# Kernel tuning notes

Hardware: AMD Instinct MI355X
Metric: run time of the kernel (lower is better)

## Reference

```python
import jax, jax.numpy as jnp
import numpy as np

B, OBS, H, M, L1, T, A = 16384, 376, 512, 8, 3, 50, 17  # L1 = num_layers - 1
LOG_SQRT_2PI = 0.5 * np.log(2.0 * np.pi).astype(np.float32)


def setup_inputs() -> dict:
    key = jax.random.key(0)
    ks = jax.random.split(key, 16)
    s = lambda fan: 1.0 / np.sqrt(fan).astype(np.float32)
    return {
        "x": jax.random.normal(ks[0], (B, OBS), jnp.float32),
        "task_idx": jax.random.randint(ks[1], (B,), 0, T, jnp.int64),
        "enc_W1": jax.random.normal(ks[2], (OBS, H), jnp.float32) * s(OBS),
        "enc_b1": jnp.zeros((H,), jnp.float32),
        "enc_W2": jax.random.normal(ks[3], (H, H), jnp.float32) * s(H),
        "enc_b2": jnp.zeros((H,), jnp.float32),
        "task_emb": jax.random.normal(ks[4], (T, H), jnp.float32),
        "a_rW": jax.random.normal(ks[5], (L1, H, M * M), jnp.float32) * s(H),
        "a_rb": jnp.zeros((L1, M * M), jnp.float32),
        "c_rW": jax.random.normal(ks[6], (L1, H, M * M), jnp.float32) * s(H),
        "c_rb": jnp.zeros((L1, M * M), jnp.float32),
        "a_W": jax.random.normal(ks[7], (L1, M, H, H), jnp.float32) * s(H),
        "a_b": jnp.zeros((L1, M, H), jnp.float32),
        "a_Wf": jax.random.normal(ks[8], (M, H, A), jnp.float32) * 0.01,
        "a_bf": jnp.zeros((M, A), jnp.float32),
        "c_W": jax.random.normal(ks[9], (L1, M, H, H), jnp.float32) * s(H),
        "c_b": jnp.zeros((L1, M, H), jnp.float32),
        "c_Wf": jax.random.normal(ks[10], (M, H, 1), jnp.float32) * s(H),
        "c_bf": jnp.zeros((M, 1), jnp.float32),
        "actor_logstd": jnp.zeros((1, A), jnp.float32),
    }


def _routing(context, rW, rb):
    # context: [B,H]; rW: [L1,H,M*M] -> list of [B,M,M] softmax routing probs
    rel = jax.nn.relu(context)
    probs = []
    for l in range(L1):
        logits = (rel @ rW[l] + rb[l]).reshape(-1, M, M)
        probs.append(jax.nn.softmax(logits, axis=2))
    return probs


def _base(f_s, probs, W, b, Wf, bf):
    # f_s: [B,H]; W: [L1,M,H,H]; Wf: [M,H,out]
    g = jnp.broadcast_to(f_s[:, None, :], (f_s.shape[0], M, H))  # [B,M,H]
    for l in range(L1):
        outs = jax.nn.relu(jnp.einsum("bmh,mhk->bmk", g, W[l]) + b[l])  # [B,M,H]
        g = jnp.einsum("bij,bjh->bih", probs[l], outs)  # soft combine
    final = jnp.einsum("bmh,mhk->bmk", g, Wf) + bf  # [B,M,out]
    return final.sum(axis=1)


def reference(x, task_idx, enc_W1, enc_b1, enc_W2, enc_b2, task_emb,
              a_rW, a_rb, c_rW, c_rb, a_W, a_b, a_Wf, a_bf,
              c_W, c_b, c_Wf, c_bf, actor_logstd):
    f_s = jnp.tanh(jnp.tanh(x @ enc_W1 + enc_b1) @ enc_W2 + enc_b2)  # [B,H]
    h_z = task_emb[task_idx]  # [B,H]
    context = f_s * h_z

    value = _base(f_s, _routing(context, c_rW, c_rb), c_W, c_b, c_Wf, c_bf)  # [B,1]
    mean = _base(f_s, _routing(context, a_rW, a_rb), a_W, a_b, a_Wf, a_bf)   # [B,A]

    # deterministic action (sample=False): action = mean
    logstd = jnp.broadcast_to(actor_logstd, mean.shape)
    log_prob = (-logstd - LOG_SQRT_2PI).sum(axis=1)          # N.log_prob(mean).sum(1)
    entropy = (0.5 + LOG_SQRT_2PI + logstd).sum(axis=1)
    # concat (action, log_prob, entropy, value) -> [B, A+3]
    return jnp.concatenate([mean, log_prob[:, None], entropy[:, None], value], axis=1)
```

## Files before the change

kernel.cpp:

```cpp
#include <hip/hip_runtime.h>
#include <hip/hip_bf16.h>

typedef float f32x4 __attribute__((ext_vector_type(4)));
typedef float f32x2 __attribute__((ext_vector_type(2)));
typedef int   i32x4 __attribute__((ext_vector_type(4)));
typedef int   i32x8 __attribute__((ext_vector_type(8)));

#define LOG_SQRT_2PI 0.91893853320467274f

static constexpr int BSZ  = 16384;
static constexpr int OBSN = 376;
static constexpr int HD   = 512;
static constexpr int NACT = 17;

__device__ __forceinline__ unsigned char f2fp8(float v) {
  return (unsigned char)(__builtin_amdgcn_cvt_pk_fp8_f32(v, v, 0, false) & 0xFF);
}

__device__ __forceinline__ void gl16(const unsigned char* g, unsigned char* l) {
  __builtin_amdgcn_global_load_lds((const __attribute__((address_space(1))) void*)g,
                                   (__attribute__((address_space(3))) void*)l, 16, 0, 0);
}

__device__ __forceinline__ void xcd_map(int id, int gx, int gy, int& bx, int& by, int& bz) {
  int p = id & 7, l = id >> 3;
  bx = l % gx;
  int g = (l / gx) * 8 + p;
  by = g % gy;
  bz = g / gy;
}


__global__ void k_cvt_pad8(const float* __restrict__ src, unsigned char* __restrict__ dst) {
  long i = (long)blockIdx.x * 256 + threadIdx.x;
  if (i >= (long)BSZ * HD) return;
  long r = i >> 9;
  int  c = (int)(i & 511);
  dst[i] = f2fp8(c < OBSN ? src[r * OBSN + c] : 0.f);
}

__global__ void k_packT8(const float* __restrict__ src, unsigned char* __restrict__ dst,
                         int K, int N, int Kpad, long sstride, long dstride, float scale) {
  __shared__ float t[32][33];
  src += (long)blockIdx.z * sstride;
  dst += (long)blockIdx.z * dstride;
  int k0 = blockIdx.y * 32, n0 = blockIdx.x * 32;
#pragma unroll
  for (int ii = 0; ii < 4; ++ii) {
    int i = ii * 8 + threadIdx.y;
    int k = k0 + i, n = n0 + threadIdx.x;
    t[i][threadIdx.x] = (k < K && n < N) ? src[(long)k * N + n] : 0.f;
  }
  __syncthreads();
#pragma unroll
  for (int ii = 0; ii < 4; ++ii) {
    int i = ii * 8 + threadIdx.y;
    int n = n0 + i, k = k0 + threadIdx.x;
    if (n < N && k < Kpad) dst[(long)n * Kpad + k] = f2fp8(scale * t[threadIdx.x][i]);
  }
}

__global__ void k_packwF(const float* __restrict__ aW, const float* __restrict__ cW,
                         unsigned char* __restrict__ dst) {
  __shared__ unsigned char sT[128 * 144];
  const int tid = threadIdx.x;
  const int z = blockIdx.z;
  const int t = blockIdx.y;
  const int ng = blockIdx.x;
  const int layer = z >> 4, zz = z & 15, net = zz >> 3, m = zz & 7;
  const float* src = (net ? aW : cW) + (long)(layer * 8 + m) * 262144;
#pragma unroll
  for (int i = 0; i < 64; ++i) {
    int lin = i * 256 + tid;
    int kl = lin >> 7, nl = lin & 127;
    float v = src[(long)(t * 128 + kl) * 512 + ng * 128 + nl];
    sT[nl * 144 + kl] = f2fp8(16.f * v);
  }
  __syncthreads();
#pragma unroll
  for (int f = 0; f < 2; ++f) {
    int fid = f * 256 + tid;
    int lane = fid & 63, nb_l = fid >> 6;
    int n_l = nb_l * 16 + (lane & 15);
    int klo = ((lane >> 4) & 3) * 32;
    uint4 lo = *(const uint4*)&sT[n_l * 144 + klo];
    uint4 hi = *(const uint4*)&sT[n_l * 144 + klo + 16];
    int nb = ng * 8 + nb_l;
    unsigned char* d = dst + ((((long)z * 4 + t) * 32 + nb) * 64 + lane) * 32;
    *(uint4*)d = lo;
    *(uint4*)(d + 16) = hi;
  }
}

__global__ void k_packmisc(const float* __restrict__ a_b, const float* __restrict__ c_b,
                           const float* __restrict__ aWf, const float* __restrict__ cWf,
                           const float* __restrict__ a_rb, const float* __restrict__ c_rb,
                           float* __restrict__ lb, unsigned char* __restrict__ dsta,
                           unsigned char* __restrict__ dstc, float* __restrict__ rb) {
  int i = blockIdx.x * 256 + threadIdx.x;
  if (i < 24576) {
    int layer = i >> 13, zz = (i >> 9) & 15, n = i & 511;
    int net = zz >> 3, m = zz & 7;
    lb[i] = (net ? a_b : c_b)[(layer * 8 + m) * 512 + n];
  } else if (i < 24576 + 131072) {
    int j = i - 24576;
    int n = j >> 12, kn = j & 4095;
    int hb = kn >> 9, rem = kn & 511, m = rem >> 6, u = kn & 63;
    int ko = m * 512 + hb * 64 + u;
    dsta[j] = (n < NACT) ? f2fp8(64.f * aWf[(long)ko * NACT + n]) : (unsigned char)0;
    dstc[j] = (n < 1)    ? f2fp8(64.f * cWf[ko])                  : (unsigned char)0;
  } else if (i < 24576 + 131072 + 384) {
    int j = i - 24576 - 131072;
    rb[j] = (j < 192) ? a_rb[j] : c_rb[j - 192];
  }
}

__global__ void k_initout2(const float* __restrict__ a_bf, const float* __restrict__ c_bf,
                           const float* __restrict__ ls, float* __restrict__ out) {
  long i = (long)blockIdx.x * 256 + threadIdx.x;
  if (i >= (long)BSZ * 20) return;
  int o = (int)(i % 20);
  float v = 0.f;
  if (o < NACT) {
    for (int m = 0; m < 8; ++m) v += a_bf[m * NACT + o];
  } else if (o == 19) {
    for (int m = 0; m < 8; ++m) v += c_bf[m];
  } else if (o == 17) {
    for (int a = 0; a < NACT; ++a) v += -ls[a] - LOG_SQRT_2PI;
  } else {
    for (int a = 0; a < NACT; ++a) v += 0.5f + LOG_SQRT_2PI + ls[a];
  }
  out[i] = v;
}

template <int OP>
__global__ __launch_bounds__(256, 4)
void k_gemm8(const unsigned char* __restrict__ A, const unsigned char* __restrict__ Bt,
             void* __restrict__ Cv, const float* __restrict__ bias,
             int N, int K, int lda, int ldc, int gx, int gy,
             const int* __restrict__ tidx, const float* __restrict__ temb,
             unsigned char* __restrict__ out2) {
  __shared__ alignas(16) unsigned char sA[128 * 128];
  __shared__ alignas(16) unsigned char sB[128 * 128];
  int bx, by, z;
  xcd_map(blockIdx.x, gx, gy, bx, by, z);
  const int tid  = threadIdx.x;
  const int wave = tid >> 6, lane = tid & 63;
  const int wr = (wave >> 1) * 64, wc = (wave & 1) * 64;
  const int row0 = by * 128, col0 = bx * 128;
  const int lcol = lane & 15, quad = lane >> 4;
  const int sw7 = lcol & 7;
  const int c0 = ((2 * quad)     ^ sw7) * 16;
  const int c1 = ((2 * quad + 1) ^ sw7) * 16;
  const int raA0 = (wr + lcol) * 128 + c0, raA1 = (wr + lcol) * 128 + c1;
  const int rbB0 = (wc + lcol) * 128 + c0, rbB1 = (wc + lcol) * 128 + c1;
  int aOff[4], bOff[4];
#pragma unroll
  for (int i = 0; i < 4; ++i) {
    int u = i * 256 + tid;
    int r = u >> 3, gc = (u & 7) ^ (r & 7);
    aOff[i] = (row0 + r) * lda + gc * 16;
    bOff[i] = (col0 + r) * K + gc * 16;
  }

  f32x4 acc[4][4] = {};

  for (int kt = 0; kt < K; kt += 128) {
#pragma unroll
    for (int i = 0; i < 4; ++i) gl16(A + aOff[i] + kt, &sA[i * 4096 + tid * 16]);
#pragma unroll
    for (int i = 0; i < 4; ++i) gl16(Bt + bOff[i] + kt, &sB[i * 4096 + tid * 16]);
    __syncthreads();
    i32x8 bv[4];
#pragma unroll
    for (int ni = 0; ni < 4; ++ni) {
      i32x4 blo = *(const i32x4*)&sB[rbB0 + ni * 2048];
      i32x4 bhi = *(const i32x4*)&sB[rbB1 + ni * 2048];
      bv[ni] = (i32x8){blo[0], blo[1], blo[2], blo[3], bhi[0], bhi[1], bhi[2], bhi[3]};
    }
#pragma unroll
    for (int mi = 0; mi < 4; ++mi) {
      i32x4 alo = *(const i32x4*)&sA[raA0 + mi * 2048];
      i32x4 ahi = *(const i32x4*)&sA[raA1 + mi * 2048];
      i32x8 af = (i32x8){alo[0], alo[1], alo[2], alo[3], ahi[0], ahi[1], ahi[2], ahi[3]};
#pragma unroll
      for (int ni = 0; ni < 4; ++ni)
        acc[mi][ni] = __builtin_amdgcn_mfma_scale_f32_16x16x128_f8f6f4(
            bv[ni], af, acc[mi][ni], 0, 0, 0, 0x7F, 0, 0x7F);
    }
    __syncthreads();
  }

#pragma unroll
  for (int ni = 0; ni < 4; ++ni) {
    int colb = col0 + wc + ni * 16 + quad * 4;
    if (colb >= N) continue;
    float4 bw = *(const float4*)&bias[colb];
#pragma unroll
    for (int mi = 0; mi < 4; ++mi) {
      int rowg = row0 + wr + mi * 16 + lcol;
      float v0 = acc[mi][ni][0] * 0.0625f + bw.x;
      float v1 = acc[mi][ni][1] * 0.0625f + bw.y;
      float v2 = acc[mi][ni][2] * 0.0625f + bw.z;
      float v3 = acc[mi][ni][3] * 0.0625f + bw.w;
      long idx = (long)rowg * ldc + colb;
      if (OP == 1) {
        float t0 = tanhf(v0), t1 = tanhf(v1), t2 = tanhf(v2), t3 = tanhf(v3);
        unsigned d = __builtin_amdgcn_cvt_pk_fp8_f32(t0, t1, 0, false);
        d = __builtin_amdgcn_cvt_pk_fp8_f32(t2, t3, d, true);
        *(unsigned*)&((unsigned char*)Cv)[idx] = d;
      } else if (OP == 5) {
        float t0 = tanhf(v0), t1 = tanhf(v1), t2 = tanhf(v2), t3 = tanhf(v3);
        unsigned d = __builtin_amdgcn_cvt_pk_fp8_f32(t0, t1, 0, false);
        d = __builtin_amdgcn_cvt_pk_fp8_f32(t2, t3, d, true);
        *(unsigned*)&((unsigned char*)Cv)[idx] = d;
        int tk = tidx[rowg];
        float4 te = *(const float4*)&temb[(long)tk * HD + colb];
        unsigned e = __builtin_amdgcn_cvt_pk_fp8_f32(fmaxf(t0 * te.x, 0.f), fmaxf(t1 * te.y, 0.f), 0, false);
        e = __builtin_amdgcn_cvt_pk_fp8_f32(fmaxf(t2 * te.z, 0.f), fmaxf(t3 * te.w, 0.f), e, true);
        *(unsigned*)&out2[idx] = e;
      } else if (OP == 4) {
        float mx = fmaxf(fmaxf(v0, v1), fmaxf(v2, v3));
        mx = fmaxf(mx, __shfl_xor(mx, 16));
        float e0 = __expf(v0 - mx), e1 = __expf(v1 - mx), e2 = __expf(v2 - mx), e3 = __expf(v3 - mx);
        float s = e0 + e1 + e2 + e3;
        s += __shfl_xor(s, 16);
        float inv = 1.f / s;
        *(float4*)&((float*)Cv)[idx] = make_float4(e0 * inv, e1 * inv, e2 * inv, e3 * inv);
      }
    }
  }
}

template <int AMODE, int HEAD>
__global__ __launch_bounds__(512, 4)
void k_gemmF(const unsigned char* __restrict__ A, const unsigned char* __restrict__ Wp,
             const float* __restrict__ lb, const float* __restrict__ probs,
             unsigned char* __restrict__ g, int gy, int poffC, int poffA,
             const unsigned char* __restrict__ Wfc, const unsigned char* __restrict__ Wfa,
             float* __restrict__ outp) {
  __shared__ alignas(16) unsigned char sL[AMODE ? 65536 : 32768];
  int hb, slab, net;
  xcd_map(blockIdx.x, 8, gy, hb, slab, net);
  const int tid = threadIdx.x;
  const int w = tid >> 6, lane = tid & 63;
  const int lcol = lane & 15, quad = lane >> 4;
  const int ln3 = lane >> 3, sl = lane & 7;
  const int row0 = slab * 64;
  const int h0 = hb * 64;
  const int sw7 = lcol & 7;
  const int c0 = ((2 * quad)     ^ sw7) * 16;
  const int c1 = ((2 * quad + 1) ^ sw7) * 16;
  const int ch = sl ^ ln3;
  const unsigned char* wbase =
      Wp + (((long)(net * 8 + w) * 4 * 32 + hb * 4) * 64 + lane) * 32;

  f32x4 acc[4][4] = {};

  if (AMODE == 0) {
#pragma unroll
    for (int i = 0; i < 4; ++i) {
      int vb = w * 4 + i;
      int rr = (vb & 7) * 8 + ln3;
      gl16(A + (row0 + rr) * 512 + (vb >> 3) * 128 + ch * 16, &sL[(vb * 64 + lane) * 16]);
    }
    __syncthreads();
#pragma unroll
    for (int t = 0; t < 4; ++t) {
      i32x8 bv[4];
#pragma unroll
      for (int ni = 0; ni < 4; ++ni) {
        i32x4 lo = *(const i32x4*)(wbase + t * 65536 + ni * 2048);
        i32x4 hi = *(const i32x4*)(wbase + t * 65536 + ni * 2048 + 16);
        bv[ni] = (i32x8){lo[0], lo[1], lo[2], lo[3], hi[0], hi[1], hi[2], hi[3]};
      }
      __builtin_amdgcn_s_setprio(1);
#pragma unroll
      for (int mi = 0; mi < 4; ++mi) {
        int ra = t * 8192 + (mi * 16 + lcol) * 128;
        i32x4 lo = *(const i32x4*)&sL[ra + c0];
        i32x4 hi = *(const i32x4*)&sL[ra + c1];
        i32x8 af = (i32x8){lo[0], lo[1], lo[2], lo[3], hi[0], hi[1], hi[2], hi[3]};
#pragma unroll
        for (int ni = 0; ni < 4; ++ni)
          acc[mi][ni] = __builtin_amdgcn_mfma_scale_f32_16x16x128_f8f6f4(
              bv[ni], af, acc[mi][ni], 0, 0, 0, 0x7F, 0, 0x7F);
      }
      __builtin_amdgcn_s_setprio(0);
    }
  } else {
    const unsigned char* abase = A + (long)(row0 + ln3) * 8192 + net * 4096 +
                                 w * 64 + (ch >> 2) * 512 + (ch & 3) * 16;
    unsigned char* dbase = &sL[w * 8192 + lane * 16];
#pragma unroll 1
    for (int t = 0; t < 4; ++t) {
#pragma unroll
      for (int i = 0; i < 8; ++i)
        gl16(abase + i * 8 * 8192 + t * 1024, dbase + i * 1024);
      i32x8 bv[4];
#pragma unroll
      for (int ni = 0; ni < 4; ++ni) {
        i32x4 lo = *(const i32x4*)(wbase + t * 65536 + ni * 2048);
        i32x4 hi = *(const i32x4*)(wbase + t * 65536 + ni * 2048 + 16);
        bv[ni] = (i32x8){lo[0], lo[1], lo[2], lo[3], hi[0], hi[1], hi[2], hi[3]};
      }
      asm volatile("s_waitcnt vmcnt(0)" ::: "memory");
      __builtin_amdgcn_sched_barrier(0);
      __builtin_amdgcn_s_setprio(1);
#pragma unroll
      for (int mi = 0; mi < 4; ++mi) {
        int ra = w * 8192 + (mi * 16 + lcol) * 128;
        i32x4 lo = *(const i32x4*)&sL[ra + c0];
        i32x4 hi = *(const i32x4*)&sL[ra + c1];
        i32x8 af = (i32x8){lo[0], lo[1], lo[2], lo[3], hi[0], hi[1], hi[2], hi[3]};
#pragma unroll
        for (int ni = 0; ni < 4; ++ni)
          acc[mi][ni] = __builtin_amdgcn_mfma_scale_f32_16x16x128_f8f6f4(
              bv[ni], af, acc[mi][ni], 0, 0, 0, 0x7F, 0, 0x7F);
      }
      __builtin_amdgcn_s_setprio(0);
    }
  }

  __syncthreads();

#pragma unroll
  for (int ni = 0; ni < 4; ++ni) {
    int col = ni * 16 + quad * 4;
    float4 bw = *(const float4*)&lb[(net * 8 + w) * 512 + h0 + col];
    int sd = ni * 4 + quad;
#pragma unroll
    for (int mi = 0; mi < 4; ++mi) {
      int row = mi * 16 + lcol;
      float v0 = fmaxf(acc[mi][ni][0] * 0.0625f + bw.x, 0.f);
      float v1 = fmaxf(acc[mi][ni][1] * 0.0625f + bw.y, 0.f);
      float v2 = fmaxf(acc[mi][ni][2] * 0.0625f + bw.z, 0.f);
      float v3 = fmaxf(acc[mi][ni][3] * 0.0625f + bw.w, 0.f);
      unsigned d = __builtin_amdgcn_cvt_pk_fp8_f32(v0, v1, 0, false);
      d = __builtin_amdgcn_cvt_pk_fp8_f32(v2, v3, d, true);
      *(unsigned*)&sL[w * 4096 + row * 64 + ((sd ^ (row & 14)) << 2)] = d;
    }
  }
  __syncthreads();

  const int poff = net ? poffA : poffC;
#pragma unroll
  for (int k = 0; k < 8; ++k) {
    const int r = k * 8 + ln3;
    const float* pr = &probs[(long)(row0 + r) * 384 + poff + w * 8];
    float4 pA = *(const float4*)pr;
    float4 pB = *(const float4*)(pr + 4);
    float p8[8] = {pA.x, pA.y, pA.z, pA.w, pB.x, pB.y, pB.z, pB.w};
    f32x2 ga2[4] = {};
#pragma unroll
    for (int j = 0; j < 8; ++j) {
      uint2 o2 = *(const uint2*)&sL[j * 4096 + r * 64 + (((sl * 2) ^ (r & 14)) << 2)];
      f32x2 pw2 = {p8[j], p8[j]};
      ga2[0] += pw2 * __builtin_amdgcn_cvt_pk_f32_fp8(o2.x, false);
      ga2[1] += pw2 * __builtin_amdgcn_cvt_pk_f32_fp8(o2.x, true);
      ga2[2] += pw2 * __builtin_amdgcn_cvt_pk_f32_fp8(o2.y, false);
      ga2[3] += pw2 * __builtin_amdgcn_cvt_pk_f32_fp8(o2.y, true);
    }
    unsigned lo = __builtin_amdgcn_cvt_pk_fp8_f32(ga2[0][0], ga2[0][1], 0, false);
    lo = __builtin_amdgcn_cvt_pk_fp8_f32(ga2[1][0], ga2[1][1], lo, true);
    unsigned hi = __builtin_amdgcn_cvt_pk_fp8_f32(ga2[2][0], ga2[2][1], 0, false);
    hi = __builtin_amdgcn_cvt_pk_fp8_f32(ga2[3][0], ga2[3][1], hi, true);
    if (HEAD) {
      *(uint2*)&sL[32768 + w * 4096 + r * 64 + (((sl * 2) ^ (r & 14)) << 2)] =
          make_uint2(lo, hi);
    } else {
      *(uint2*)&g[(long)(row0 + r) * 8192 + net * 4096 + hb * 512 + w * 64 + sl * 8] =
          make_uint2(lo, hi);
    }
  }

  if (HEAD) {
    __syncthreads();
    const unsigned char* Wf = net ? Wfa : Wfc;
    const int ooff = net ? 0 : 19;
    const int mi = w & 3, kh = w >> 2;
    const int hrow = mi * 16 + lcol;
    f32x4 hacc[2] = {};
#pragma unroll
    for (int ks = 0; ks < 8; ++ks) {
      int j = kh * 4 + (ks >> 1);
      int u = (ks & 1) * 32 + quad * 8;
      int sd = u >> 2;
      long af = *(const long*)&sL[32768 + j * 4096 + hrow * 64 + ((sd ^ (hrow & 14)) << 2)];
      int kglob = hb * 512 + kh * 256 + ks * 32 + quad * 8;
      long bv0 = *(const long*)&Wf[(long)lcol * 4096 + kglob];
      hacc[0] = __builtin_amdgcn_mfma_f32_16x16x32_fp8_fp8(af, bv0, hacc[0], 0, 0, 0);
      if (net) {
        long bv1 = *(const long*)&Wf[(long)(16 + lcol) * 4096 + kglob];
        hacc[1] = __builtin_amdgcn_mfma_f32_16x16x32_fp8_fp8(af, bv1, hacc[1], 0, 0, 0);
      }
    }
    const int NOUTn = net ? NACT : 1;
#pragma unroll
    for (int ni = 0; ni < 2; ++ni) {
      if (ni == 1 && !net) break;
      int col = ni * 16 + lcol;
      if (col >= NOUTn) continue;
#pragma unroll
      for (int rr = 0; rr < 4; ++rr) {
        int row = row0 + mi * 16 + quad * 4 + rr;
        atomicAdd(&outp[(long)row * 20 + ooff + col], hacc[ni][rr] * 0.015625f);
      }
    }
  }
}


extern "C" void kernel_launch(void* const* d_in, const int* in_sizes, int n_in,
                              void* d_out, int out_size, void* d_ws, size_t ws_size,
                              hipStream_t stream) {
  const float* x        = (const float*)d_in[0];
  const int*   task_idx = (const int*)d_in[1];
  const float* enc_W1   = (const float*)d_in[2];
  const float* enc_b1   = (const float*)d_in[3];
  const float* enc_W2   = (const float*)d_in[4];
  const float* enc_b2   = (const float*)d_in[5];
  const float* task_emb = (const float*)d_in[6];
  const float* a_rW     = (const float*)d_in[7];
  const float* a_rb     = (const float*)d_in[8];
  const float* c_rW     = (const float*)d_in[9];
  const float* c_rb     = (const float*)d_in[10];
  const float* a_W      = (const float*)d_in[11];
  const float* a_b      = (const float*)d_in[12];
  const float* a_Wf     = (const float*)d_in[13];
  const float* a_bf     = (const float*)d_in[14];
  const float* c_W      = (const float*)d_in[15];
  const float* c_b      = (const float*)d_in[16];
  const float* c_Wf     = (const float*)d_in[17];
  const float* c_bf     = (const float*)d_in[18];
  const float* logstd   = (const float*)d_in[19];
  float* out = (float*)d_out;

  char* ws = (char*)d_ws;
  size_t off = 0;
  auto carve = [&](size_t bytes) {
    char* p = ws + off;
    off += (bytes + 255) & ~(size_t)255;
    return p;
  };
  unsigned char* W8 = (unsigned char*)carve((size_t)48 * 262144);
  unsigned char* W1T8 = (unsigned char*)carve((size_t)512 * 512);
  unsigned char* W2T8 = (unsigned char*)carve((size_t)512 * 512);
  unsigned char* rWT8 = (unsigned char*)carve((size_t)384 * 512);
  float* rball = (float*)carve(384 * 4);
  float* lb    = (float*)carve(3 * 16 * 512 * 4);
  unsigned char* WfaT8 = (unsigned char*)carve((size_t)32 * 4096);
  unsigned char* WfcT8 = (unsigned char*)carve((size_t)32 * 4096);
  unsigned char* fs8 = (unsigned char*)carve((size_t)BSZ * HD);
  float* lgt   = (float*)carve((size_t)BSZ * 384 * 4);

  size_t remain = (ws_size > off) ? (ws_size - off) : 0;
  int Bc = 2048;
  for (int cand = BSZ; cand > 2048; cand >>= 1)
    if ((size_t)2 * cand * 8192 <= remain) { Bc = cand; break; }
  size_t half = (size_t)Bc * 8192;
  unsigned char* bufA8 = (unsigned char*)carve(half);
  unsigned char* bufB8 = (unsigned char*)carve(half);
  unsigned char* x8   = bufA8;
  unsigned char* h18  = bufB8;
  unsigned char* rel8 = bufA8;

  dim3 tb(32, 8);

  k_cvt_pad8<<<(int)(((long)BSZ * HD + 255) / 256), 256, 0, stream>>>(x, x8);
  k_packT8<<<dim3(16, 16, 1), tb, 0, stream>>>(enc_W1, W1T8, OBSN, 512, 512, 0, 0, 16.f);
  k_packT8<<<dim3(16, 16, 1), tb, 0, stream>>>(enc_W2, W2T8, 512, 512, 512, 0, 0, 16.f);
  k_packT8<<<dim3(2, 16, 3),  tb, 0, stream>>>(a_rW, rWT8,             512, 64, 512, 512 * 64, 64 * 512, 16.f);
  k_packT8<<<dim3(2, 16, 3),  tb, 0, stream>>>(c_rW, rWT8 + 192 * 512, 512, 64, 512, 512 * 64, 64 * 512, 16.f);
  k_packwF<<<dim3(4, 4, 48), 256, 0, stream>>>(a_W, c_W, W8);
  k_packmisc<<<610, 256, 0, stream>>>(a_b, c_b, a_Wf, c_Wf, a_rb, c_rb,
                                      lb, WfaT8, WfcT8, rball);
  k_initout2<<<(int)(((long)BSZ * 20 + 255) / 256), 256, 0, stream>>>(a_bf, c_bf, logstd, out);

  const int GY = BSZ / 128;
  k_gemm8<1><<<4 * GY, 256, 0, stream>>>(x8, W1T8, h18, enc_b1, 512, 512, 512, 512,
                                         4, GY, nullptr, nullptr, nullptr);
  k_gemm8<5><<<4 * GY, 256, 0, stream>>>(h18, W2T8, fs8, enc_b2, 512, 512, 512, 512,
                                         4, GY, task_idx, task_emb, rel8);
  k_gemm8<4><<<3 * GY, 256, 0, stream>>>(rel8, rWT8, lgt, rball, 384, 512, 512, 384,
                                         3, GY, nullptr, nullptr, nullptr);

  const size_t wlz = (size_t)16 * 262144;
  for (int c0 = 0; c0 < BSZ; c0 += Bc) {
    const unsigned char* fs_c = fs8 + (long)c0 * 512;
    const float* pr_c  = lgt + (long)c0 * 384;
    float*       out_c = out + (long)c0 * 20;
    const int gyF = Bc / 64;

    k_gemmF<0, 0><<<16 * gyF, 512, 0, stream>>>(fs_c, W8, lb, pr_c, bufA8, gyF, 192, 0,
                                                nullptr, nullptr, nullptr);
    k_gemmF<1, 0><<<16 * gyF, 512, 0, stream>>>(bufA8, W8 + wlz, lb + 8192, pr_c, bufB8,
                                                gyF, 192 + 64, 64, nullptr, nullptr, nullptr);
    k_gemmF<1, 1><<<16 * gyF, 512, 0, stream>>>(bufB8, W8 + 2 * wlz, lb + 16384, pr_c, bufA8,
                                                gyF, 192 + 128, 128, WfcT8, WfaT8, out_c);
  }
}
```

Before: 696.7 us.

## Halve row slab for later mixture layers to raise occupancy and change g layout

For layers 2 and 3 of the mixture network, each block now handles 32 rows instead of 64. This halves the LDS footprint to 32 KB and the accumulator registers, and the launch bound is raised to 6 blocks per CU so more waves stay resident. The intermediate g buffer layout changes from hb*512 + w*64 to w*512 + h0, making each expert's hidden vector contiguous so the layer loads become 128-byte contiguous chunks per expert. The trade-off is twice as many blocks and weight fetches per row, so each weight byte is reused less.

```diff
diff --git a/kernel.cpp b/kernel.cpp
--- a/kernel.cpp
+++ b/kernel.cpp
@@ -233,20 +233,20 @@
 }
 
 template <int AMODE, int HEAD>
-__global__ __launch_bounds__(512, 4)
+__global__ __launch_bounds__(512, AMODE ? 6 : 4)
 void k_gemmF(const unsigned char* __restrict__ A, const unsigned char* __restrict__ Wp,
              const float* __restrict__ lb, const float* __restrict__ probs,
              unsigned char* __restrict__ g, int gy, int poffC, int poffA,
              const unsigned char* __restrict__ Wfc, const unsigned char* __restrict__ Wfa,
              float* __restrict__ outp) {
-  __shared__ alignas(16) unsigned char sL[AMODE ? 65536 : 32768];
+  __shared__ alignas(16) unsigned char sL[32768];
   int hb, slab, net;
   xcd_map(blockIdx.x, 8, gy, hb, slab, net);
   const int tid = threadIdx.x;
   const int w = tid >> 6, lane = tid & 63;
   const int lcol = lane & 15, quad = lane >> 4;
   const int ln3 = lane >> 3, sl = lane & 7;
-  const int row0 = slab * 64;
+  const int row0 = slab * (AMODE ? 32 : 64);
   const int h0 = hb * 64;
   const int sw7 = lcol & 7;
   const int c0 = ((2 * quad)     ^ sw7) * 16;
@@ -254,10 +254,10 @@
   const int ch = sl ^ ln3;
   const unsigned char* wbase =
       Wp + (((long)(net * 8 + w) * 4 * 32 + hb * 4) * 64 + lane) * 32;
-
-  f32x4 acc[4][4] = {};
+  const int poff = net ? poffA : poffC;
 
   if (AMODE == 0) {
+    f32x4 acc[4][4] = {};
 #pragma unroll
     for (int i = 0; i < 4; ++i) {
       int vb = w * 4 + i;
@@ -288,40 +288,88 @@
       }
       __builtin_amdgcn_s_setprio(0);
     }
-  } else {
+    __syncthreads();
+
+#pragma unroll
+    for (int ni = 0; ni < 4; ++ni) {
+      int col = ni * 16 + quad * 4;
+      float4 bw = *(const float4*)&lb[(net * 8 + w) * 512 + h0 + col];
+      int sd = ni * 4 + quad;
+#pragma unroll
+      for (int mi = 0; mi < 4; ++mi) {
+        int row = mi * 16 + lcol;
+        float v0 = fmaxf(acc[mi][ni][0] * 0.0625f + bw.x, 0.f);
+        float v1 = fmaxf(acc[mi][ni][1] * 0.0625f + bw.y, 0.f);
+        float v2 = fmaxf(acc[mi][ni][2] * 0.0625f + bw.z, 0.f);
+        float v3 = fmaxf(acc[mi][ni][3] * 0.0625f + bw.w, 0.f);
+        unsigned d = __builtin_amdgcn_cvt_pk_fp8_f32(v0, v1, 0, false);
+        d = __builtin_amdgcn_cvt_pk_fp8_f32(v2, v3, d, true);
+        *(unsigned*)&sL[w * 4096 + row * 64 + ((sd ^ (row & 14)) << 2)] = d;
+      }
+    }
+    __syncthreads();
+
+#pragma unroll
+    for (int k = 0; k < 8; ++k) {
+      const int r = k * 8 + ln3;
+      const float* pr = &probs[(long)(row0 + r) * 384 + poff + w * 8];
+      float4 pA = *(const float4*)pr;
+      float4 pB = *(const float4*)(pr + 4);
+      float p8[8] = {pA.x, pA.y, pA.z, pA.w, pB.x, pB.y, pB.z, pB.w};
+      f32x2 ga2[4] = {};
+#pragma unroll
+      for (int j = 0; j < 8; ++j) {
+        uint2 o2 = *(const uint2*)&sL[j * 4096 + r * 64 + (((sl * 2) ^ (r & 14)) << 2)];
+        f32x2 pw2 = {p8[j], p8[j]};
+        ga2[0] += pw2 * __builtin_amdgcn_cvt_pk_f32_fp8(o2.x, false);
+        ga2[1] += pw2 * __builtin_amdgcn_cvt_pk_f32_fp8(o2.x, true);
+        ga2[2] += pw2 * __builtin_amdgcn_cvt_pk_f32_fp8(o2.y, false);
+        ga2[3] += pw2 * __builtin_amdgcn_cvt_pk_f32_fp8(o2.y, true);
+      }
+      unsigned lo = __builtin_amdgcn_cvt_pk_fp8_f32(ga2[0][0], ga2[0][1], 0, false);
+      lo = __builtin_amdgcn_cvt_pk_fp8_f32(ga2[1][0], ga2[1][1], lo, true);
+      unsigned hi = __builtin_amdgcn_cvt_pk_fp8_f32(ga2[2][0], ga2[2][1], 0, false);
+      hi = __builtin_amdgcn_cvt_pk_fp8_f32(ga2[3][0], ga2[3][1], hi, true);
+      *(uint2*)&g[(long)(row0 + r) * 8192 + net * 4096 + w * 512 + h0 + sl * 8] =
+          make_uint2(lo, hi);
+    }
+    return;
+  }
+
+  f32x4 acc[2][4] = {};
+  {
     const unsigned char* abase = A + (long)(row0 + ln3) * 8192 + net * 4096 +
-                                 w * 64 + (ch >> 2) * 512 + (ch & 3) * 16;
-    unsigned char* dbase = &sL[w * 8192 + lane * 16];
+                                 w * 512 + ch * 16;
+    unsigned char* dbase = &sL[w * 4096 + lane * 16];
 #pragma unroll 1
     for (int t = 0; t < 4; ++t) {
 #pragma unroll
-      for (int i = 0; i < 8; ++i)
-        gl16(abase + i * 8 * 8192 + t * 1024, dbase + i * 1024);
-      i32x8 bv[4];
+      for (int i = 0; i < 4; ++i)
+        gl16(abase + i * 8 * 8192 + t * 128, dbase + i * 1024);
+      asm volatile("s_waitcnt vmcnt(0)" ::: "memory");
+      __builtin_amdgcn_sched_barrier(0);
+      i32x8 af[2];
+#pragma unroll
+      for (int mi = 0; mi < 2; ++mi) {
+        int ra = w * 4096 + (mi * 16 + lcol) * 128;
+        i32x4 lo = *(const i32x4*)&sL[ra + c0];
+        i32x4 hi = *(const i32x4*)&sL[ra + c1];
+        af[mi] = (i32x8){lo[0], lo[1], lo[2], lo[3], hi[0], hi[1], hi[2], hi[3]};
+      }
+      __builtin_amdgcn_s_setprio(1);
 #pragma unroll
       for (int ni = 0; ni < 4; ++ni) {
         i32x4 lo = *(const i32x4*)(wbase + t * 65536 + ni * 2048);
         i32x4 hi = *(const i32x4*)(wbase + t * 65536 + ni * 2048 + 16);
-        bv[ni] = (i32x8){lo[0], lo[1], lo[2], lo[3], hi[0], hi[1], hi[2], hi[3]};
-      }
-      asm volatile("s_waitcnt vmcnt(0)" ::: "memory");
-      __builtin_amdgcn_sched_barrier(0);
-      __builtin_amdgcn_s_setprio(1);
-#pragma unroll
-      for (int mi = 0; mi < 4; ++mi) {
-        int ra = w * 8192 + (mi * 16 + lcol) * 128;
-        i32x4 lo = *(const i32x4*)&sL[ra + c0];
-        i32x4 hi = *(const i32x4*)&sL[ra + c1];
-        i32x8 af = (i32x8){lo[0], lo[1], lo[2], lo[3], hi[0], hi[1], hi[2], hi[3]};
-#pragma unroll
-        for (int ni = 0; ni < 4; ++ni)
-          acc[mi][ni] = __builtin_amdgcn_mfma_scale_f32_16x16x128_f8f6f4(
-              bv[ni], af, acc[mi][ni], 0, 0, 0, 0x7F, 0, 0x7F);
+        i32x8 bv = (i32x8){lo[0], lo[1], lo[2], lo[3], hi[0], hi[1], hi[2], hi[3]};
+        acc[0][ni] = __builtin_amdgcn_mfma_scale_f32_16x16x128_f8f6f4(
+            bv, af[0], acc[0][ni], 0, 0, 0, 0x7F, 0, 0x7F);
+        acc[1][ni] = __builtin_amdgcn_mfma_scale_f32_16x16x128_f8f6f4(
+            bv, af[1], acc[1][ni], 0, 0, 0, 0x7F, 0, 0x7F);
       }
       __builtin_amdgcn_s_setprio(0);
     }
   }
-
   __syncthreads();
 
 #pragma unroll
@@ -330,7 +378,7 @@
     float4 bw = *(const float4*)&lb[(net * 8 + w) * 512 + h0 + col];
     int sd = ni * 4 + quad;
 #pragma unroll
-    for (int mi = 0; mi < 4; ++mi) {
+    for (int mi = 0; mi < 2; ++mi) {
       int row = mi * 16 + lcol;
       float v0 = fmaxf(acc[mi][ni][0] * 0.0625f + bw.x, 0.f);
       float v1 = fmaxf(acc[mi][ni][1] * 0.0625f + bw.y, 0.f);
@@ -338,14 +386,13 @@
       float v3 = fmaxf(acc[mi][ni][3] * 0.0625f + bw.w, 0.f);
       unsigned d = __builtin_amdgcn_cvt_pk_fp8_f32(v0, v1, 0, false);
       d = __builtin_amdgcn_cvt_pk_fp8_f32(v2, v3, d, true);
-      *(unsigned*)&sL[w * 4096 + row * 64 + ((sd ^ (row & 14)) << 2)] = d;
+      *(unsigned*)&sL[w * 2048 + row * 64 + ((sd ^ (row & 14)) << 2)] = d;
     }
   }
   __syncthreads();
 
-  const int poff = net ? poffA : poffC;
-#pragma unroll
-  for (int k = 0; k < 8; ++k) {
+#pragma unroll
+  for (int k = 0; k < 4; ++k) {
     const int r = k * 8 + ln3;
     const float* pr = &probs[(long)(row0 + r) * 384 + poff + w * 8];
     float4 pA = *(const float4*)pr;
@@ -354,7 +401,7 @@
     f32x2 ga2[4] = {};
 #pragma unroll
     for (int j = 0; j < 8; ++j) {
-      uint2 o2 = *(const uint2*)&sL[j * 4096 + r * 64 + (((sl * 2) ^ (r & 14)) << 2)];
+      uint2 o2 = *(const uint2*)&sL[j * 2048 + r * 64 + (((sl * 2) ^ (r & 14)) << 2)];
       f32x2 pw2 = {p8[j], p8[j]};
       ga2[0] += pw2 * __builtin_amdgcn_cvt_pk_f32_fp8(o2.x, false);
       ga2[1] += pw2 * __builtin_amdgcn_cvt_pk_f32_fp8(o2.x, true);
@@ -366,10 +413,10 @@
     unsigned hi = __builtin_amdgcn_cvt_pk_fp8_f32(ga2[2][0], ga2[2][1], 0, false);
     hi = __builtin_amdgcn_cvt_pk_fp8_f32(ga2[3][0], ga2[3][1], hi, true);
     if (HEAD) {
-      *(uint2*)&sL[32768 + w * 4096 + r * 64 + (((sl * 2) ^ (r & 14)) << 2)] =
+      *(uint2*)&sL[16384 + w * 2048 + r * 64 + (((sl * 2) ^ (r & 14)) << 2)] =
           make_uint2(lo, hi);
     } else {
-      *(uint2*)&g[(long)(row0 + r) * 8192 + net * 4096 + hb * 512 + w * 64 + sl * 8] =
+      *(uint2*)&g[(long)(row0 + r) * 8192 + net * 4096 + w * 512 + h0 + sl * 8] =
           make_uint2(lo, hi);
     }
   }
@@ -378,16 +425,16 @@
     __syncthreads();
     const unsigned char* Wf = net ? Wfa : Wfc;
     const int ooff = net ? 0 : 19;
-    const int mi = w & 3, kh = w >> 2;
+    const int mi = w & 1, kq = w >> 1;
     const int hrow = mi * 16 + lcol;
     f32x4 hacc[2] = {};
 #pragma unroll
-    for (int ks = 0; ks < 8; ++ks) {
-      int j = kh * 4 + (ks >> 1);
+    for (int ks = 0; ks < 4; ++ks) {
+      int j = kq * 2 + (ks >> 1);
       int u = (ks & 1) * 32 + quad * 8;
       int sd = u >> 2;
-      long af = *(const long*)&sL[32768 + j * 4096 + hrow * 64 + ((sd ^ (hrow & 14)) << 2)];
-      int kglob = hb * 512 + kh * 256 + ks * 32 + quad * 8;
+      long af = *(const long*)&sL[16384 + j * 2048 + hrow * 64 + ((sd ^ (hrow & 14)) << 2)];
+      int kglob = hb * 512 + j * 64 + u;
       long bv0 = *(const long*)&Wf[(long)lcol * 4096 + kglob];
       hacc[0] = __builtin_amdgcn_mfma_f32_16x16x32_fp8_fp8(af, bv0, hacc[0], 0, 0, 0);
       if (net) {
@@ -490,13 +537,13 @@
     const unsigned char* fs_c = fs8 + (long)c0 * 512;
     const float* pr_c  = lgt + (long)c0 * 384;
     float*       out_c = out + (long)c0 * 20;
-    const int gyF = Bc / 64;
-
-    k_gemmF<0, 0><<<16 * gyF, 512, 0, stream>>>(fs_c, W8, lb, pr_c, bufA8, gyF, 192, 0,
+    const int gy1 = Bc / 64, gy2 = Bc / 32;
+
+    k_gemmF<0, 0><<<16 * gy1, 512, 0, stream>>>(fs_c, W8, lb, pr_c, bufA8, gy1, 192, 0,
                                                 nullptr, nullptr, nullptr);
-    k_gemmF<1, 0><<<16 * gyF, 512, 0, stream>>>(bufA8, W8 + wlz, lb + 8192, pr_c, bufB8,
-                                                gyF, 192 + 64, 64, nullptr, nullptr, nullptr);
-    k_gemmF<1, 1><<<16 * gyF, 512, 0, stream>>>(bufB8, W8 + 2 * wlz, lb + 16384, pr_c, bufA8,
-                                                gyF, 192 + 128, 128, WfcT8, WfaT8, out_c);
-  }
-}
+    k_gemmF<1, 0><<<16 * gy2, 512, 0, stream>>>(bufA8, W8 + wlz, lb + 8192, pr_c, bufB8,
+                                                gy2, 192 + 64, 64, nullptr, nullptr, nullptr);
+    k_gemmF<1, 1><<<16 * gy2, 512, 0, stream>>>(bufB8, W8 + 2 * wlz, lb + 16384, pr_c, bufA8,
+                                                gy2, 192 + 128, 128, WfcT8, WfaT8, out_c);
+  }
+}
```

Result: slower. 798.8 us (+14.6%).
